# Kernel tuning notes

Hardware: AMD Instinct MI355X
Metric: run time of the kernel (lower is better)

Reference implementation:

```python
import jax, jax.numpy as jnp
import numpy as np

HIDDEN = 1024
HEADS = 16
HEAD_SIZE = HIDDEN // HEADS


def setup_inputs() -> dict:
    key = jax.random.key(0)
    k0, k1, k2, k3 = jax.random.split(key, 4)
    scale = 1.0 / np.sqrt(HIDDEN)
    return {
        "input_data": jax.random.normal(k0, (4, 4096, HIDDEN), dtype=jnp.float32),
        "W0": jax.random.normal(k1, (HIDDEN, HIDDEN), dtype=jnp.float32) * scale,
        "W1": jax.random.normal(k2, (HIDDEN, HIDDEN), dtype=jnp.float32) * scale,
        "W2": jax.random.normal(k3, (HIDDEN, HIDDEN), dtype=jnp.float32) * scale,
    }


def reference(input_data, W0, W1, W2):
    b, s, _ = input_data.shape
    k, h = HEADS, HEAD_SIZE
    # torch.nn.Linear(bias=False): y = x @ W.T
    out = input_data @ W0.T          # [b, s, hidden]
    out1 = input_data @ W1.T
    out2 = input_data @ W2.T
    # reshape to heads; cummax over the sequence axis (axis=1 here, which
    # matches cummax(dim=2) on the permuted (b,k,s,h) layout in torch)
    out_h = out.reshape(b, s, k, h)
    out1_h = out1.reshape(b, s, k, h)
    cm = jax.lax.associative_scan(jnp.maximum, (out_h + out1_h) / jnp.sqrt(jnp.float32(h)), axis=1)
    cm = cm.reshape(b, s, k * h)
    out = (cm + out2) * cm + out1
    return out
```

## Files before the change

kernel.cpp:

```cpp
#include <hip/hip_runtime.h>
#include <cstdint>
#include <cstddef>

#define HIDDEN 1024
#define BATCH 4
#define SEQ 4096
#define M_ROWS (BATCH * SEQ)
#define K_DIM 1024
#define SUBCHUNK 32
#define NSUB (SEQ / SUBCHUNK)

typedef __bf16 bf16_t;
typedef __bf16 v8bf __attribute__((ext_vector_type(8)));
typedef float v4f __attribute__((ext_vector_type(4)));
typedef unsigned short us8 __attribute__((ext_vector_type(8)));

__device__ __forceinline__ unsigned short f32_to_bf16(float f) {
  unsigned int u = __float_as_uint(f);
  u += 0x7fffu + ((u >> 16) & 1u);
  return (unsigned short)(u >> 16);
}
__device__ __forceinline__ float bf16_to_f32(unsigned short u) {
  return __uint_as_float((unsigned int)u << 16);
}

__global__ void convert_kernel(const float* __restrict__ X,
                               const float* __restrict__ W0,
                               const float* __restrict__ W1,
                               const float* __restrict__ W2,
                               unsigned short* __restrict__ Xb,
                               unsigned short* __restrict__ Wb) {
  int bx = blockIdx.x;
  if (bx < 16384) {
    int i = bx * 256 + threadIdx.x;
    float4 f = ((const float4*)X)[i];
    ushort4 u;
    u.x = f32_to_bf16(f.x); u.y = f32_to_bf16(f.y);
    u.z = f32_to_bf16(f.z); u.w = f32_to_bf16(f.w);
    ((ushort4*)Xb)[i] = u;
  } else {
    int i = (bx - 16384) * 256 + threadIdx.x;
    int mat = i >> 18;
    int off = i & 0x3FFFF;
    float4 f;
    if (mat == 0) {
      float4 a = ((const float4*)W0)[off];
      float4 b = ((const float4*)W1)[off];
      f.x = (a.x + b.x) * 0.125f; f.y = (a.y + b.y) * 0.125f;
      f.z = (a.z + b.z) * 0.125f; f.w = (a.w + b.w) * 0.125f;
    } else {
      const float* src = (mat == 1) ? W1 : W2;
      f = ((const float4*)src)[off];
    }
    ushort4 u;
    u.x = f32_to_bf16(f.x); u.y = f32_to_bf16(f.y);
    u.z = f32_to_bf16(f.z); u.w = f32_to_bf16(f.w);
    ((ushort4*)Wb)[i] = u;
  }
}

__global__ __launch_bounds__(512, 2) void gemm_s_kernel(
    const bf16_t* __restrict__ A, const bf16_t* __restrict__ B,
    unsigned short* __restrict__ Lp, float* __restrict__ cmax) {
  extern __shared__ __align__(16) char smem[];

  const int tid = threadIdx.x;
  const int wave = tid >> 6;
  const int lane = tid & 63;
  const int quad = lane >> 4;
  const int r16 = lane & 15;
  const int wr = wave >> 2;
  const int wc = wave & 3;

  const int orig = (int)blockIdx.x;
  const int swz = (orig & 7) * 32 + (orig >> 3);
  const int bx = swz & 3;
  const int mt = swz >> 2;
  const int mtile0 = mt * 256;
  const int nbase = bx * 256;

  const int l3 = lane >> 3;
  const int lc = lane & 7;
  const size_t laneOff = (size_t)l3 * K_DIM + (size_t)((lc ^ l3) << 3);
  const bf16_t* Ag = A + (size_t)(mtile0 + wave * 8) * K_DIM + laneOff;
  const bf16_t* Bg = B + (size_t)(nbase + wave * 8) * K_DIM + laneOff;

  const int aRow = (wr * 128 + r16) * 128;
  const int bRow = (wc * 64 + r16) * 128;
  const int cxor = (r16 & 7) * 16;
  const int qx = quad * 16;

  v4f acc[8][4];
#pragma unroll
  for (int i = 0; i < 8; ++i)
#pragma unroll
    for (int j = 0; j < 4; ++j) acc[i][j] = (v4f)(0.0f);

  v8bf afrE[4], afrO[4];
  v8bf bfr[4][2];

#define STG_A(d, q, kt) __builtin_amdgcn_global_load_lds( \
    (__attribute__((address_space(1))) void*)(Ag + (size_t)(q) * (64 * K_DIM) + (size_t)(kt) * 64), \
    (__attribute__((address_space(3))) void*)(smem + (d) * 32768 + (q) * 8192 + wave * 1024), 16, 0, 0)
#define STG_B(d, q, kt) __builtin_amdgcn_global_load_lds( \
    (__attribute__((address_space(1))) void*)(Bg + (size_t)(q) * (64 * K_DIM) + (size_t)(kt) * 64), \
    (__attribute__((address_space(3))) void*)(smem + 65536 + (d) * 32768 + (q) * 8192 + wave * 1024), 16, 0, 0)
#define LDA(d, i, kk) (*(const v8bf*)(smem + (d) * 32768 + aRow + (i) * 2048 + (((kk) * 64 + qx) ^ cxor)))
#define LDB(d, j, kk) (*(const v8bf*)(smem + 65536 + (d) * 32768 + bRow + (j) * 2048 + (((kk) * 64 + qx) ^ cxor)))
#define RD_AE(d, ih, kk) { _Pragma("unroll") for (int ii = 0; ii < 4; ++ii) afrE[ii] = LDA(d, (ih) * 4 + ii, kk); }
#define RD_AO(d, ih, kk) { _Pragma("unroll") for (int ii = 0; ii < 4; ++ii) afrO[ii] = LDA(d, (ih) * 4 + ii, kk); }
#define RD_B(d, kk) { _Pragma("unroll") for (int j = 0; j < 4; ++j) bfr[j][kk] = LDB(d, j, kk); }
#define MMS(AF, ih, kk) \
  __builtin_amdgcn_s_setprio(1); \
  { _Pragma("unroll") for (int ii = 0; ii < 4; ++ii) { _Pragma("unroll") for (int j = 0; j < 4; ++j) \
      acc[(ih) * 4 + ii][j] = __builtin_amdgcn_mfma_f32_16x16x32_bf16(AF[ii], bfr[j][(kk)], acc[(ih) * 4 + ii][j], 0, 0, 0); } } \
  __builtin_amdgcn_s_setprio(0);
#define BAR() __builtin_amdgcn_s_barrier()
#define WAITV(n) asm volatile("s_waitcnt vmcnt(" #n ")" ::: "memory")

  STG_A(0, 0, 0); STG_A(0, 1, 0); STG_A(0, 2, 0); STG_A(0, 3, 0);
  STG_B(0, 0, 0); STG_B(0, 1, 0); STG_B(0, 2, 0); STG_B(0, 3, 0);
  STG_A(1, 0, 1); STG_A(1, 2, 1); STG_B(1, 0, 1); STG_B(1, 1, 1);
  WAITV(4);
  BAR();
  RD_AE(0, 0, 0); RD_B(0, 0);

  for (int it = 0; it < 7; ++it) {
    const int t1 = 2 * it + 1, t2 = t1 + 1, t3 = t1 + 2;
    STG_B(1, 2, t1); STG_B(1, 3, t1);
    BAR();
    RD_B(0, 1); RD_AO(0, 0, 1);
    MMS(afrE, 0, 0); BAR();
    STG_A(1, 1, t1); STG_A(1, 3, t1);
    BAR();
    RD_AE(0, 1, 0);
    MMS(afrO, 0, 1); BAR();
    STG_A(0, 0, t2); STG_A(0, 2, t2);
    BAR();
    RD_AO(0, 1, 1);
    MMS(afrE, 1, 0); BAR();
    STG_B(0, 0, t2); STG_B(0, 1, t2);
    BAR();
    WAITV(4); BAR();
    RD_AE(1, 0, 0); RD_B(1, 0);
    MMS(afrO, 1, 1); BAR();
    STG_B(0, 2, t2); STG_B(0, 3, t2);
    BAR();
    RD_B(1, 1); RD_AO(1, 0, 1);
    MMS(afrE, 0, 0); BAR();
    STG_A(0, 1, t2); STG_A(0, 3, t2);
    BAR();
    RD_AE(1, 1, 0);
    MMS(afrO, 0, 1); BAR();
    STG_A(1, 0, t3); STG_A(1, 2, t3);
    BAR();
    RD_AO(1, 1, 1);
    MMS(afrE, 1, 0); BAR();
    STG_B(1, 0, t3); STG_B(1, 1, t3);
    BAR();
    WAITV(4); BAR();
    RD_AE(0, 0, 0); RD_B(0, 0);
    MMS(afrO, 1, 1); BAR();
  }
  STG_B(1, 2, 15); STG_B(1, 3, 15);
  BAR();
  RD_B(0, 1); RD_AO(0, 0, 1);
  MMS(afrE, 0, 0); BAR();
  STG_A(1, 1, 15); STG_A(1, 3, 15);
  BAR();
  RD_AE(0, 1, 0);
  MMS(afrO, 0, 1); BAR();
  RD_AO(0, 1, 1);
  MMS(afrE, 1, 0); BAR();
  WAITV(0); BAR();
  RD_AE(1, 0, 0); RD_B(1, 0);
  MMS(afrO, 1, 1); BAR();
  RD_B(1, 1); RD_AO(1, 0, 1);
  MMS(afrE, 0, 0); BAR();
  RD_AE(1, 1, 0);
  MMS(afrO, 0, 1); BAR();
  RD_AO(1, 1, 1);
  MMS(afrE, 1, 0); BAR();
  MMS(afrO, 1, 1);

#undef STG_A
#undef STG_B
#undef LDA
#undef LDB
#undef RD_AE
#undef RD_AO
#undef RD_B
#undef MMS
#undef BAR
#undef WAITV

  const int ncol0 = bx * 256;
  const int bidx = mtile0 >> 12;
  const int sub0 = (mtile0 & 4095) >> 5;
#pragma unroll
  for (int s = 0; s < 4; ++s) {
#pragma unroll
    for (int j = 0; j < 4; ++j) {
      float c0[4], c1[4];
      c0[0] = acc[s * 2][j][0];
      c1[0] = acc[s * 2 + 1][j][0];
#pragma unroll
      for (int r = 1; r < 4; ++r) {
        c0[r] = fmaxf(c0[r - 1], acc[s * 2][j][r]);
        c1[r] = fmaxf(c1[r - 1], acc[s * 2 + 1][j][r]);
      }
      float t0 = c0[3], t1 = c1[3], u;
      u = __shfl_up(t0, 16); if (quad >= 1) t0 = fmaxf(t0, u);
      u = __shfl_up(t0, 32); if (quad >= 2) t0 = fmaxf(t0, u);
      u = __shfl_up(t1, 16); if (quad >= 1) t1 = fmaxf(t1, u);
      u = __shfl_up(t1, 32); if (quad >= 2) t1 = fmaxf(t1, u);
      float e0 = __shfl_up(t0, 16); if (quad == 0) e0 = -INFINITY;
      float e1 = __shfl_up(t1, 16); if (quad == 0) e1 = -INFINITY;
      float T0 = __shfl(t0, 48 + r16);
      float T1 = __shfl(t1, 48 + r16);
      int col = ncol0 + wc * 64 + j * 16 + r16;
      int rowb = mtile0 + wr * 128 + s * 32 + quad * 4;
#pragma unroll
      for (int r = 0; r < 4; ++r) {
        float L0 = fmaxf(c0[r], e0);
        float L1 = fmaxf(fmaxf(c1[r], e1), T0);
        Lp[(size_t)(rowb + r) * HIDDEN + col] = f32_to_bf16(L0);
        Lp[(size_t)(rowb + 16 + r) * HIDDEN + col] = f32_to_bf16(L1);
      }
      if (quad == 0) {
        int sub = sub0 + wr * 4 + s;
        cmax[((size_t)bidx * NSUB + sub) * HIDDEN + col] = fmaxf(T0, T1);
      }
    }
  }
}

__global__ void prefix_kernel(const float* __restrict__ cmax,
                              float* __restrict__ pmax) {
  int col = blockIdx.x * 256 + threadIdx.x;
  int b = blockIdx.y;
  const float* cp = cmax + (size_t)b * NSUB * HIDDEN + col;
  float* pp = pmax + (size_t)b * NSUB * HIDDEN + col;
  float run = -INFINITY;
#pragma unroll 1
  for (int s0 = 0; s0 < NSUB; s0 += 16) {
    float v[16];
#pragma unroll
    for (int i = 0; i < 16; ++i) v[i] = cp[(size_t)(s0 + i) * HIDDEN];
#pragma unroll
    for (int i = 0; i < 16; ++i) {
      pp[(size_t)(s0 + i) * HIDDEN] = run;
      run = fmaxf(run, v[i]);
    }
  }
}

__global__ __launch_bounds__(512, 2) void gemm_f_kernel(
    const bf16_t* __restrict__ A, const bf16_t* __restrict__ B,
    const unsigned short* __restrict__ Lp, const float* __restrict__ pmax,
    float* __restrict__ out) {
  extern __shared__ __align__(16) char smem[];

  const int tid = threadIdx.x;
  const int wave = tid >> 6;
  const int lane = tid & 63;
  const int quad = lane >> 4;
  const int r16 = lane & 15;
  const int wr = wave >> 2;
  const int wc = wave & 3;

  const int orig = (int)blockIdx.x;
  const int swz = (orig & 7) * 64 + (orig >> 3);
  const int mt = swz >> 3;
  const int nt = swz & 7;
  const int mtile0 = mt * 256;
  const int ncol0 = nt * 128;

  const int l3 = lane >> 3;
  const int lc = lane & 7;
  const size_t laneOff = (size_t)l3 * K_DIM + (size_t)((lc ^ l3) << 3);
  const bf16_t* Ag = A + (size_t)(mtile0 + wave * 8) * K_DIM + laneOff;
  const bf16_t* Bg1 = B + (size_t)(1024 + ncol0 + wave * 8) * K_DIM + laneOff;
  const bf16_t* Bg2 = B + (size_t)(2048 + ncol0 + wave * 8) * K_DIM + laneOff;

  const int aRow = (wr * 128 + r16) * 128;
  const int bRow = (wc * 32 + r16) * 128;
  const int cxor = (r16 & 7) * 16;
  const int qx = quad * 16;

  v4f acc1[8][2], acc2[8][2];
#pragma unroll
  for (int i = 0; i < 8; ++i)
#pragma unroll
    for (int j = 0; j < 2; ++j) { acc1[i][j] = (v4f)(0.0f); acc2[i][j] = (v4f)(0.0f); }

  v8bf afrE[4], afrO[4];
  v8bf b1fr[2][2], b2fr[2][2];

#define STG2_A(d, q, kt) __builtin_amdgcn_global_load_lds( \
    (__attribute__((address_space(1))) void*)(Ag + (size_t)(q) * (64 * K_DIM) + (size_t)(kt) * 64), \
    (__attribute__((address_space(3))) void*)(smem + (d) * 32768 + (q) * 8192 + wave * 1024), 16, 0, 0)
#define STG2_B1(d, q, kt) __builtin_amdgcn_global_load_lds( \
    (__attribute__((address_space(1))) void*)(Bg1 + (size_t)(q) * (64 * K_DIM) + (size_t)(kt) * 64), \
    (__attribute__((address_space(3))) void*)(smem + 65536 + (d) * 32768 + (q) * 8192 + wave * 1024), 16, 0, 0)
#define STG2_B2(d, q, kt) __builtin_amdgcn_global_load_lds( \
    (__attribute__((address_space(1))) void*)(Bg2 + (size_t)(q) * (64 * K_DIM) + (size_t)(kt) * 64), \
    (__attribute__((address_space(3))) void*)(smem + 65536 + (d) * 32768 + 16384 + (q) * 8192 + wave * 1024), 16, 0, 0)
#define LDA2(d, i, kk) (*(const v8bf*)(smem + (d) * 32768 + aRow + (i) * 2048 + (((kk) * 64 + qx) ^ cxor)))
#define LDB21(d, j, kk) (*(const v8bf*)(smem + 65536 + (d) * 32768 + bRow + (j) * 2048 + (((kk) * 64 + qx) ^ cxor)))
#define LDB22(d, j, kk) (*(const v8bf*)(smem + 65536 + (d) * 32768 + 16384 + bRow + (j) * 2048 + (((kk) * 64 + qx) ^ cxor)))
#define RD2_AE(d, ih, kk) { _Pragma("unroll") for (int ii = 0; ii < 4; ++ii) afrE[ii] = LDA2(d, (ih) * 4 + ii, kk); }
#define RD2_AO(d, ih, kk) { _Pragma("unroll") for (int ii = 0; ii < 4; ++ii) afrO[ii] = LDA2(d, (ih) * 4 + ii, kk); }
#define RD2_B(d, kk) { _Pragma("unroll") for (int j = 0; j < 2; ++j) { b1fr[j][kk] = LDB21(d, j, kk); b2fr[j][kk] = LDB22(d, j, kk); } }
#define MMS2(AF, ih, kk) \
  __builtin_amdgcn_s_setprio(1); \
  { _Pragma("unroll") for (int ii = 0; ii < 4; ++ii) { _Pragma("unroll") for (int j = 0; j < 2; ++j) { \
      acc1[(ih) * 4 + ii][j] = __builtin_amdgcn_mfma_f32_16x16x32_bf16(AF[ii], b1fr[j][(kk)], acc1[(ih) * 4 + ii][j], 0, 0, 0); \
      acc2[(ih) * 4 + ii][j] = __builtin_amdgcn_mfma_f32_16x16x32_bf16(AF[ii], b2fr[j][(kk)], acc2[(ih) * 4 + ii][j], 0, 0, 0); } } } \
  __builtin_amdgcn_s_setprio(0);
#define BAR() __builtin_amdgcn_s_barrier()
#define WAITV(n) asm volatile("s_waitcnt vmcnt(" #n ")" ::: "memory")

  STG2_A(0, 0, 0); STG2_A(0, 1, 0); STG2_A(0, 2, 0); STG2_A(0, 3, 0);
  STG2_B1(0, 0, 0); STG2_B1(0, 1, 0); STG2_B2(0, 0, 0); STG2_B2(0, 1, 0);
  STG2_A(1, 0, 1); STG2_A(1, 2, 1); STG2_B1(1, 0, 1); STG2_B1(1, 1, 1);
  WAITV(4);
  BAR();
  RD2_AE(0, 0, 0); RD2_B(0, 0);

  for (int it = 0; it < 7; ++it) {
    const int t1 = 2 * it + 1, t2 = t1 + 1, t3 = t1 + 2;
    STG2_B2(1, 0, t1); STG2_B2(1, 1, t1);
    BAR();
    RD2_B(0, 1); RD2_AO(0, 0, 1);
    MMS2(afrE, 0, 0); BAR();
    STG2_A(1, 1, t1); STG2_A(1, 3, t1);
    BAR();
    RD2_AE(0, 1, 0);
    MMS2(afrO, 0, 1); BAR();
    STG2_A(0, 0, t2); STG2_A(0, 2, t2);
    BAR();
    RD2_AO(0, 1, 1);
    MMS2(afrE, 1, 0); BAR();
    STG2_B1(0, 0, t2); STG2_B1(0, 1, t2);
    BAR();
    WAITV(4); BAR();
    RD2_AE(1, 0, 0); RD2_B(1, 0);
    MMS2(afrO, 1, 1); BAR();
    STG2_B2(0, 0, t2); STG2_B2(0, 1, t2);
    BAR();
    RD2_B(1, 1); RD2_AO(1, 0, 1);
    MMS2(afrE, 0, 0); BAR();
    STG2_A(0, 1, t2); STG2_A(0, 3, t2);
    BAR();
    RD2_AE(1, 1, 0);
    MMS2(afrO, 0, 1); BAR();
    STG2_A(1, 0, t3); STG2_A(1, 2, t3);
    BAR();
    RD2_AO(1, 1, 1);
    MMS2(afrE, 1, 0); BAR();
    STG2_B1(1, 0, t3); STG2_B1(1, 1, t3);
    BAR();
    WAITV(4); BAR();
    RD2_AE(0, 0, 0); RD2_B(0, 0);
    MMS2(afrO, 1, 1); BAR();
  }
  STG2_B2(1, 0, 15); STG2_B2(1, 1, 15);
  BAR();
  RD2_B(0, 1); RD2_AO(0, 0, 1);
  MMS2(afrE, 0, 0); BAR();
  STG2_A(1, 1, 15); STG2_A(1, 3, 15);
  BAR();
  RD2_AE(0, 1, 0);
  MMS2(afrO, 0, 1); BAR();
  RD2_AO(0, 1, 1);
  MMS2(afrE, 1, 0); BAR();
  WAITV(0); BAR();
  RD2_AE(1, 0, 0); RD2_B(1, 0);
  MMS2(afrO, 1, 1); BAR();
  RD2_B(1, 1); RD2_AO(1, 0, 1);
  MMS2(afrE, 0, 0); BAR();
  RD2_AE(1, 1, 0);
  MMS2(afrO, 0, 1); BAR();
  RD2_AO(1, 1, 1);
  MMS2(afrE, 1, 0); BAR();
  MMS2(afrO, 1, 1);

#undef STG2_A
#undef STG2_B1
#undef STG2_B2
#undef LDA2
#undef LDB21
#undef LDB22
#undef RD2_AE
#undef RD2_AO
#undef RD2_B
#undef MMS2
#undef BAR
#undef WAITV

  const int bidx = mtile0 >> 12;
  const int sub0 = (mtile0 & 4095) >> 5;
#pragma unroll
  for (int i = 0; i < 8; ++i) {
    const int subr = sub0 + wr * 4 + (i >> 1);
#pragma unroll
    for (int j = 0; j < 2; ++j) {
      const int col = ncol0 + wc * 32 + j * 16 + r16;
      const float pm = pmax[((size_t)bidx * NSUB + subr) * HIDDEN + col];
      const int row0 = mtile0 + wr * 128 + i * 16 + quad * 4;
#pragma unroll
      for (int r = 0; r < 4; ++r) {
        size_t idx = (size_t)(row0 + r) * HIDDEN + col;
        float m = fmaxf(pm, bf16_to_f32(Lp[idx]));
        out[idx] = (m + acc2[i][j][r]) * m + acc1[i][j][r];
      }
    }
  }
}

extern "C" void kernel_launch(void* const* d_in, const int* in_sizes, int n_in,
                              void* d_out, int out_size, void* d_ws, size_t ws_size,
                              hipStream_t stream) {
  const float* X = (const float*)d_in[0];
  const float* W0 = (const float*)d_in[1];
  const float* W1 = (const float*)d_in[2];
  const float* W2 = (const float*)d_in[3];
  float* out = (float*)d_out;

  char* ws = (char*)d_ws;
  unsigned short* Xb = (unsigned short*)ws;
  unsigned short* Wb = (unsigned short*)(ws + 33554432);
  unsigned short* Lp = (unsigned short*)(ws + 33554432 + 6291456);
  float* cmax = (float*)(ws + 4 * 33554432 + 6291456);
  float* pmax = (float*)(ws + 4 * 33554432 + 6291456 + 2097152);

  convert_kernel<<<19456, 256, 0, stream>>>(X, W0, W1, W2, Xb, Wb);

  gemm_s_kernel<<<256, 512, 131072, stream>>>((const bf16_t*)Xb, (const bf16_t*)Wb,
                                              Lp, cmax);

  dim3 pgrid(4, BATCH);
  prefix_kernel<<<pgrid, 256, 0, stream>>>(cmax, pmax);

  gemm_f_kernel<<<512, 512, 131072, stream>>>((const bf16_t*)Xb, (const bf16_t*)Wb,
                                              Lp, pmax, out);
}
```

Baseline: 131.3 us.

## Store local cummax in fragment-tiled layout and prefetch it before GEMM tail

```diff
diff --git a/kernel.cpp b/kernel.cpp
--- a/kernel.cpp
+++ b/kernel.cpp
@@ -59,9 +59,10 @@
   }
 }
 
+
 __global__ __launch_bounds__(512, 2) void gemm_s_kernel(
     const bf16_t* __restrict__ A, const bf16_t* __restrict__ B,
-    unsigned short* __restrict__ Lp, float* __restrict__ cmax) {
+    unsigned short* __restrict__ Lf, float* __restrict__ cmax) {
   extern __shared__ __align__(16) char smem[];
 
   const int tid = threadIdx.x;
@@ -197,8 +198,10 @@
   const int ncol0 = bx * 256;
   const int bidx = mtile0 >> 12;
   const int sub0 = (mtile0 & 4095) >> 5;
+  const int slot = (quad * 16 + r16) * 4;
 #pragma unroll
   for (int s = 0; s < 4; ++s) {
+    const int rT0 = (mtile0 + wr * 128 + s * 32) >> 4;
 #pragma unroll
     for (int j = 0; j < 4; ++j) {
       float c0[4], c1[4];
@@ -218,17 +221,22 @@
       float e1 = __shfl_up(t1, 16); if (quad == 0) e1 = -INFINITY;
       float T0 = __shfl(t0, 48 + r16);
       float T1 = __shfl(t1, 48 + r16);
-      int col = ncol0 + wc * 64 + j * 16 + r16;
-      int rowb = mtile0 + wr * 128 + s * 32 + quad * 4;
-#pragma unroll
-      for (int r = 0; r < 4; ++r) {
-        float L0 = fmaxf(c0[r], e0);
-        float L1 = fmaxf(fmaxf(c1[r], e1), T0);
-        Lp[(size_t)(rowb + r) * HIDDEN + col] = f32_to_bf16(L0);
-        Lp[(size_t)(rowb + 16 + r) * HIDDEN + col] = f32_to_bf16(L1);
-      }
+      const int cT = (ncol0 + wc * 64 + j * 16) >> 4;
+      ushort4 p0, p1;
+      p0.x = f32_to_bf16(fmaxf(c0[0], e0));
+      p0.y = f32_to_bf16(fmaxf(c0[1], e0));
+      p0.z = f32_to_bf16(fmaxf(c0[2], e0));
+      p0.w = f32_to_bf16(fmaxf(c0[3], e0));
+      float f1 = fmaxf(e1, T0);
+      p1.x = f32_to_bf16(fmaxf(c1[0], f1));
+      p1.y = f32_to_bf16(fmaxf(c1[1], f1));
+      p1.z = f32_to_bf16(fmaxf(c1[2], f1));
+      p1.w = f32_to_bf16(fmaxf(c1[3], f1));
+      *(ushort4*)(Lf + ((size_t)rT0 * 64 + cT) * 256 + slot) = p0;
+      *(ushort4*)(Lf + ((size_t)(rT0 + 1) * 64 + cT) * 256 + slot) = p1;
       if (quad == 0) {
         int sub = sub0 + wr * 4 + s;
+        int col = ncol0 + wc * 64 + j * 16 + r16;
         cmax[((size_t)bidx * NSUB + sub) * HIDDEN + col] = fmaxf(T0, T1);
       }
     }
@@ -257,7 +265,7 @@
 
 __global__ __launch_bounds__(512, 2) void gemm_f_kernel(
     const bf16_t* __restrict__ A, const bf16_t* __restrict__ B,
-    const unsigned short* __restrict__ Lp, const float* __restrict__ pmax,
+    const unsigned short* __restrict__ Lf, const float* __restrict__ pmax,
     float* __restrict__ out) {
   extern __shared__ __align__(16) char smem[];
 
@@ -365,6 +373,26 @@
     RD2_AE(0, 0, 0); RD2_B(0, 0);
     MMS2(afrO, 1, 1); BAR();
   }
+
+  const int bidx = mtile0 >> 12;
+  const int sub0 = (mtile0 & 4095) >> 5;
+  const int rTbase = (mtile0 + wr * 128) >> 4;
+  const int cTbase = (ncol0 + wc * 32) >> 4;
+  const int slot = (quad * 16 + r16) * 4;
+  ushort4 lfv[8][2];
+  float pmv[4][2];
+#pragma unroll
+  for (int i = 0; i < 8; ++i)
+#pragma unroll
+    for (int j = 0; j < 2; ++j)
+      lfv[i][j] = *(const ushort4*)(Lf + ((size_t)(rTbase + i) * 64 + cTbase + j) * 256 + slot);
+#pragma unroll
+  for (int s4 = 0; s4 < 4; ++s4)
+#pragma unroll
+    for (int j = 0; j < 2; ++j)
+      pmv[s4][j] = pmax[((size_t)bidx * NSUB + sub0 + wr * 4 + s4) * HIDDEN
+                        + ncol0 + wc * 32 + j * 16 + r16];
+
   STG2_B2(1, 0, 15); STG2_B2(1, 1, 15);
   BAR();
   RD2_B(0, 1); RD2_AO(0, 0, 1);
@@ -399,22 +427,26 @@
 #undef BAR
 #undef WAITV
 
-  const int bidx = mtile0 >> 12;
-  const int sub0 = (mtile0 & 4095) >> 5;
 #pragma unroll
   for (int i = 0; i < 8; ++i) {
-    const int subr = sub0 + wr * 4 + (i >> 1);
-#pragma unroll
-    for (int j = 0; j < 2; ++j) {
-      const int col = ncol0 + wc * 32 + j * 16 + r16;
-      const float pm = pmax[((size_t)bidx * NSUB + subr) * HIDDEN + col];
-      const int row0 = mtile0 + wr * 128 + i * 16 + quad * 4;
-#pragma unroll
-      for (int r = 0; r < 4; ++r) {
-        size_t idx = (size_t)(row0 + r) * HIDDEN + col;
-        float m = fmaxf(pm, bf16_to_f32(Lp[idx]));
-        out[idx] = (m + acc2[i][j][r]) * m + acc1[i][j][r];
-      }
+    const int row0 = mtile0 + wr * 128 + i * 16 + quad * 4;
+    const int colb = ncol0 + wc * 32 + r16;
+    const float pmA = pmv[i >> 1][0], pmB = pmv[i >> 1][1];
+    const ushort4 lA = lfv[i][0], lB = lfv[i][1];
+    float mA[4], mB[4];
+    mA[0] = fmaxf(pmA, bf16_to_f32(lA.x));
+    mA[1] = fmaxf(pmA, bf16_to_f32(lA.y));
+    mA[2] = fmaxf(pmA, bf16_to_f32(lA.z));
+    mA[3] = fmaxf(pmA, bf16_to_f32(lA.w));
+    mB[0] = fmaxf(pmB, bf16_to_f32(lB.x));
+    mB[1] = fmaxf(pmB, bf16_to_f32(lB.y));
+    mB[2] = fmaxf(pmB, bf16_to_f32(lB.z));
+    mB[3] = fmaxf(pmB, bf16_to_f32(lB.w));
+#pragma unroll
+    for (int r = 0; r < 4; ++r) {
+      size_t idx = (size_t)(row0 + r) * HIDDEN + colb;
+      out[idx] = (mA[r] + acc2[i][0][r]) * mA[r] + acc1[i][0][r];
+      out[idx + 16] = (mB[r] + acc2[i][1][r]) * mB[r] + acc1[i][1][r];
     }
   }
 }
@@ -431,18 +463,18 @@
   char* ws = (char*)d_ws;
   unsigned short* Xb = (unsigned short*)ws;
   unsigned short* Wb = (unsigned short*)(ws + 33554432);
-  unsigned short* Lp = (unsigned short*)(ws + 33554432 + 6291456);
+  unsigned short* Lf = (unsigned short*)(ws + 33554432 + 6291456);
   float* cmax = (float*)(ws + 4 * 33554432 + 6291456);
   float* pmax = (float*)(ws + 4 * 33554432 + 6291456 + 2097152);
 
   convert_kernel<<<19456, 256, 0, stream>>>(X, W0, W1, W2, Xb, Wb);
 
   gemm_s_kernel<<<256, 512, 131072, stream>>>((const bf16_t*)Xb, (const bf16_t*)Wb,
-                                              Lp, cmax);
+                                              Lf, cmax);
 
   dim3 pgrid(4, BATCH);
   prefix_kernel<<<pgrid, 256, 0, stream>>>(cmax, pmax);
 
   gemm_f_kernel<<<512, 512, 131072, stream>>>((const bf16_t*)Xb, (const bf16_t*)Wb,
-                                              Lp, pmax, out);
-}
+                                              Lf, pmax, out);
+}
```

After: 133.7 us. No clear change (+1.8%).
